# Kernel optimization log

Hardware: AMD Instinct MI355X
Metric: run time of the kernel (lower is better)

The kernel has to match this reference:

```python
import jax, jax.numpy as jnp
import numpy as np

B, S, D = 2, 2048, 1024
NH, HD = 16, 64
MLP = 4096
EPS = 1e-6  # flax nnx.RMSNorm default epsilon


def rms_norm(x, scale):
    var = jnp.mean(jnp.square(x.astype(jnp.float32)), axis=-1, keepdims=True)
    return (x * jax.lax.rsqrt(var + EPS)).astype(x.dtype) * scale


def setup_inputs() -> dict:
    key = jax.random.key(0)
    ks = jax.random.split(key, 16)
    lin = lambda k, fin, fout: jax.random.normal(k, (fin, fout), jnp.float32) / np.sqrt(fin)
    x = jax.random.normal(ks[0], (B, S, D), jnp.float32)
    # causal mask [b, s, s]
    mask = jnp.broadcast_to(jnp.tril(jnp.ones((S, S), jnp.bool_))[None], (B, S, S))
    return {
        "x": x,
        "mask": mask,
        "attn_norm_scale": jnp.ones((D,), jnp.float32),
        "q_w": lin(ks[1], D, D), "q_b": jnp.zeros((D,), jnp.float32),
        "k_w": lin(ks[2], D, D), "k_b": jnp.zeros((D,), jnp.float32),
        "v_w": lin(ks[3], D, D), "v_b": jnp.zeros((D,), jnp.float32),
        "o_w": lin(ks[4], D, D), "o_b": jnp.zeros((D,), jnp.float32),
        "ffn_norm_scale": jnp.ones((D,), jnp.float32),
        "gate_w": lin(ks[5], D, MLP), "gate_b": jnp.zeros((MLP,), jnp.float32),
        "up_w": lin(ks[6], D, MLP), "up_b": jnp.zeros((MLP,), jnp.float32),
        "down_w": lin(ks[7], MLP, D), "down_b": jnp.zeros((D,), jnp.float32),
    }


def reference(x, mask, attn_norm_scale, q_w, q_b, k_w, k_b, v_w, v_b, o_w, o_b,
              ffn_norm_scale, gate_w, gate_b, up_w, up_b, down_w, down_b):
    b, s, d = x.shape
    h = rms_norm(x, attn_norm_scale)
    q = (h @ q_w + q_b).reshape(b, s, NH, HD)
    k = (h @ k_w + k_b).reshape(b, s, NH, HD)
    v = (h @ v_w + v_b).reshape(b, s, NH, HD)
    scale = jnp.float32(HD) ** -0.5
    logits = jnp.einsum('bsnh,btnh->bnst', q, k) * scale  # [b, n, s, s]
    logits = jnp.where(mask[:, None, :, :], logits, jnp.finfo(logits.dtype).min)
    attn = jax.nn.softmax(logits.astype(jnp.float32), axis=-1).astype(x.dtype)
    attn_out = jnp.einsum('bnst,btnh->bsnh', attn, v).reshape(b, s, d)
    x = x + attn_out @ o_w + o_b
    h = rms_norm(x, ffn_norm_scale)
    ffn = (jax.nn.silu(h @ gate_w + gate_b) * (h @ up_w + up_b)) @ down_w + down_b
    return x + ffn
```

## Files before the change

kernel.cpp:

```cpp
#include <hip/hip_runtime.h>

#define S_LEN 2048
#define DMODEL 1024
#define NHEADS 16
#define MLPDIM 4096

typedef float f32x4 __attribute__((ext_vector_type(4)));
typedef __bf16 bf16x8 __attribute__((ext_vector_type(8)));
typedef __bf16 bf16x4 __attribute__((ext_vector_type(4)));

__device__ __forceinline__ void gload_lds16(const void* gsrc, void* ldst) {
  __builtin_amdgcn_global_load_lds(
      (const __attribute__((address_space(1))) void*)gsrc,
      (__attribute__((address_space(3))) void*)ldst, 16, 0, 0);
}

#define BARR() __builtin_amdgcn_s_barrier()
#define LGKM0() do { asm volatile("s_waitcnt lgkmcnt(0)" ::: "memory"); __builtin_amdgcn_sched_barrier(0); } while (0)
#define VMC(n) do { asm volatile("s_waitcnt vmcnt(" #n ")" ::: "memory"); __builtin_amdgcn_sched_barrier(0); } while (0)

__global__ __launch_bounds__(256) void transpose_cast64_k(
    const float* __restrict__ in, __bf16* __restrict__ out, int K, int N) {
  __shared__ __bf16 tile[64][66];
  int n0 = blockIdx.x * 64, k0 = blockIdx.y * 64;
  int t = threadIdx.x;
  int rr = (t & 63) >> 4, sl = t & 15, wv = t >> 6;
#pragma unroll
  for (int j = 0; j < 4; ++j) {
    int r = wv * 4 + rr + j * 16;
    f32x4 v = *(const f32x4*)(in + (size_t)(k0 + r) * N + n0 + sl * 4);
#pragma unroll
    for (int e = 0; e < 4; ++e) tile[r][sl * 4 + e] = (__bf16)v[e];
  }
  __syncthreads();
#pragma unroll
  for (int j = 0; j < 2; ++j) {
    int u = t + j * 256;
    int n = u >> 3, kc = u & 7;
    bf16x8 o;
#pragma unroll
    for (int e = 0; e < 8; ++e) o[e] = tile[kc * 8 + e][n];
    *(bf16x8*)(out + (size_t)(n0 + n) * K + k0 + kc * 8) = o;
  }
}

__global__ __launch_bounds__(256) void vtrans_k(
    const __bf16* __restrict__ qkv, __bf16* __restrict__ vt) {
  __shared__ __bf16 tile[32][33];
  int s0 = blockIdx.x * 32, c0 = blockIdx.y * 32, b = blockIdx.z;
  int tx = threadIdx.x & 31, ty = threadIdx.x >> 5;
#pragma unroll
  for (int r = 0; r < 32; r += 8)
    tile[r + ty][tx] = qkv[(size_t)(b * S_LEN + s0 + r + ty) * 3072 + 2048 + c0 + tx];
  __syncthreads();
#pragma unroll
  for (int r = 0; r < 32; r += 8)
    vt[(size_t)(b * 1024 + c0 + r + ty) * S_LEN + s0 + tx] = tile[tx][r + ty];
}

__global__ __launch_bounds__(256) void concat3_k(
    const float* __restrict__ a, const float* __restrict__ b,
    const float* __restrict__ c, float* __restrict__ dst) {
  int i = blockIdx.x * 256 + threadIdx.x;
  if (i < 1024) dst[i] = a[i];
  else if (i < 2048) dst[i] = b[i - 1024];
  else if (i < 3072) dst[i] = c[i - 2048];
}

__global__ __launch_bounds__(256) void rmsnorm_k(
    const float* __restrict__ x, const float* __restrict__ scale,
    __bf16* __restrict__ out) {
  int row = blockIdx.x, tid = threadIdx.x;
  f32x4 v = ((const f32x4*)(x + (size_t)row * DMODEL))[tid];
  float ss = v[0] * v[0] + v[1] * v[1] + v[2] * v[2] + v[3] * v[3];
#pragma unroll
  for (int off = 1; off < 64; off <<= 1) ss += __shfl_xor(ss, off, 64);
  __shared__ float part[4];
  if ((tid & 63) == 0) part[tid >> 6] = ss;
  __syncthreads();
  float tot = part[0] + part[1] + part[2] + part[3];
  float r = rsqrtf(tot * (1.0f / DMODEL) + 1e-6f);
  f32x4 s4 = ((const f32x4*)scale)[tid];
  bf16x4 o;
#pragma unroll
  for (int e = 0; e < 4; ++e) o[e] = (__bf16)(v[e] * r * s4[e]);
  ((bf16x4*)out)[(size_t)row * (DMODEL / 4) + tid] = o;
}

template <int OUT_BF16, int RESID, int SILU>
__global__ __launch_bounds__(512, 2) void gemm256(
    const __bf16* __restrict__ A, const __bf16* __restrict__ Bt,
    const float* __restrict__ bias, const float* __restrict__ resid,
    const __bf16* __restrict__ aux, void* __restrict__ Cout,
    int M, int N, int K) {
  __shared__ __attribute__((aligned(16))) __bf16 smA[2][256 * 32];
  __shared__ __attribute__((aligned(16))) __bf16 smB[2][256 * 32];
  int tid = threadIdx.x, lane = tid & 63, wave = tid >> 6;
  int l15 = lane & 15, g4 = lane >> 4;
  int wr = wave >> 2, wc = wave & 3;
  int lin = blockIdx.y * gridDim.x + blockIdx.x;
  int xcd = lin & 7, idx = lin >> 3;
  int bxl = idx >> 3, byl = idx & 7;
  int bn = ((xcd & 3) * 3 + bxl) * 256;
  int bm = ((xcd >> 2) * 8 + byl) * 256;
  const char* Ab = (const char*)(A + (size_t)bm * K);
  const char* Bb = (const char*)(Bt + (size_t)bn * K);
  int NT = K >> 5;

  f32x4 acc[8][4] = {};

  int o0 = tid * 16, o1 = tid * 16 + 8192;
  int r0s = o0 >> 6, c0s = o0 & 63;
  int r1s = o1 >> 6, c1s = o1 & 63;
  int cs0 = c0s ^ (((r0s >> 1) & 3) << 4);
  int cs1 = c1s ^ (((r1s >> 1) & 3) << 4);
  size_t K2 = (size_t)K * 2;

  auto stageA = [&](int t) {
    int b2 = t & 1;
    const char* g = Ab + (size_t)t * 64;
    gload_lds16(g + (size_t)r0s * K2 + cs0, (char*)&smA[b2][0] + o0);
    gload_lds16(g + (size_t)r1s * K2 + cs1, (char*)&smA[b2][0] + o1);
  };
  auto stageB = [&](int t) {
    int b2 = t & 1;
    const char* g = Bb + (size_t)t * 64;
    gload_lds16(g + (size_t)r0s * K2 + cs0, (char*)&smB[b2][0] + o0);
    gload_lds16(g + (size_t)r1s * K2 + cs1, (char*)&smB[b2][0] + o1);
  };
  auto rdA = [&](int b2, int r) -> bf16x8 {
    return *(const bf16x8*)((const char*)&smA[b2][0] + r * 64 + ((16 * g4) ^ (((r >> 1) & 3) << 4)));
  };
  auto rdB = [&](int b2, int r) -> bf16x8 {
    return *(const bf16x8*)((const char*)&smB[b2][0] + r * 64 + ((16 * g4) ^ (((r >> 1) & 3) << 4)));
  };

  stageA(0);
  stageB(0);
  stageB(1);
  VMC(2);
  BARR();

  for (int t = 0; t < NT; ++t) {
    int b2 = t & 1;
    bf16x8 af[4], bfr[4];
#pragma unroll
    for (int m = 0; m < 4; ++m) af[m] = rdA(b2, wr * 128 + m * 16 + l15);
#pragma unroll
    for (int n = 0; n < 4; ++n) bfr[n] = rdB(b2, wc * 64 + n * 16 + l15);
    if (t + 1 < NT) stageA(t + 1);
    BARR();
    LGKM0();
    __builtin_amdgcn_s_setprio(1);
#pragma unroll
    for (int m = 0; m < 4; ++m)
#pragma unroll
      for (int n = 0; n < 4; ++n)
        acc[m][n] = __builtin_amdgcn_mfma_f32_16x16x32_bf16(af[m], bfr[n], acc[m][n], 0, 0, 0);
    __builtin_amdgcn_s_setprio(0);
    BARR();
#pragma unroll
    for (int m = 0; m < 4; ++m) af[m] = rdA(b2, wr * 128 + 64 + m * 16 + l15);
    if (t + 2 < NT) stageB(t + 2);
    BARR();
    LGKM0();
    __builtin_amdgcn_s_setprio(1);
#pragma unroll
    for (int m = 0; m < 4; ++m)
#pragma unroll
      for (int n = 0; n < 4; ++n)
        acc[4 + m][n] = __builtin_amdgcn_mfma_f32_16x16x32_bf16(af[m], bfr[n], acc[4 + m][n], 0, 0, 0);
    __builtin_amdgcn_s_setprio(0);
    if (t < NT - 2) { VMC(2); }
    else if (t == NT - 2) { VMC(0); }
    BARR();
  }

  int r0 = bm + wr * 128 + g4 * 4;
  int c0 = bn + wc * 64 + l15;
#pragma unroll
  for (int n = 0; n < 4; ++n) {
    int c = c0 + n * 16;
    float bv = bias[c];
#pragma unroll
    for (int m = 0; m < 8; ++m) {
      int rb = r0 + m * 16;
#pragma unroll
      for (int rg = 0; rg < 4; ++rg) {
        int r = rb + rg;
        size_t idx2 = (size_t)r * N + c;
        float v = acc[m][n][rg] + bv;
        if (SILU) {
          float gg = (float)aux[idx2];
          v *= gg / (1.0f + __expf(-gg));
        }
        if (RESID) v += resid[idx2];
        if (OUT_BF16) ((__bf16*)Cout)[idx2] = (__bf16)v;
        else ((float*)Cout)[idx2] = v;
      }
    }
  }
}

__global__ __launch_bounds__(256, 4) void gemm_gu(
    const __bf16* __restrict__ A, const __bf16* __restrict__ Gt,
    const __bf16* __restrict__ Ut, const float* __restrict__ gb,
    const float* __restrict__ ub, __bf16* __restrict__ Cout,
    int M, int N, int K) {
  __shared__ __attribute__((aligned(16))) __bf16 As[128 * 64];
  __shared__ __attribute__((aligned(16))) __bf16 Gs[64 * 64];
  __shared__ __attribute__((aligned(16))) __bf16 Us[64 * 64];
  int tid = threadIdx.x, lane = tid & 63, wave = tid >> 6;
  int l15 = lane & 15, g4 = lane >> 4;
  int lin = blockIdx.x;
  int xcd = lin & 7, idx = lin >> 3;
  int bxl = idx >> 4, byl = idx & 15;
  int bn = ((xcd & 3) * 16 + bxl) * 64;
  int bm = ((xcd >> 2) * 16 + byl) * 128;
  int wr = wave >> 1, wc = wave & 1;
  f32x4 ag[4][2] = {}, au[4][2] = {};
  const __bf16* Abase = A + (size_t)bm * K;
  const __bf16* Gbase = Gt + (size_t)bn * K;
  const __bf16* Ubase = Ut + (size_t)bn * K;

  for (int k0 = 0; k0 < K; k0 += 64) {
#pragma unroll
    for (int j = 0; j < 4; ++j) {
      int u = tid + j * 256;
      int r = u >> 3, c = (u & 7) ^ (r & 7);
      gload_lds16(Abase + (size_t)r * K + k0 + c * 8, As + u * 8);
    }
#pragma unroll
    for (int j = 0; j < 2; ++j) {
      int u = tid + j * 256;
      int r = u >> 3, c = (u & 7) ^ (r & 7);
      gload_lds16(Gbase + (size_t)r * K + k0 + c * 8, Gs + u * 8);
      gload_lds16(Ubase + (size_t)r * K + k0 + c * 8, Us + u * 8);
    }
    __syncthreads();
#pragma unroll
    for (int ks = 0; ks < 2; ++ks) {
      bf16x8 af[4], gf[2], uf[2];
#pragma unroll
      for (int m = 0; m < 4; ++m) {
        int r = wr * 64 + m * 16 + l15;
        af[m] = *(const bf16x8*)(As + r * 64 + (((4 * ks + g4) ^ (r & 7)) << 3));
      }
#pragma unroll
      for (int n = 0; n < 2; ++n) {
        int r = wc * 32 + n * 16 + l15;
        int off = r * 64 + (((4 * ks + g4) ^ (r & 7)) << 3);
        gf[n] = *(const bf16x8*)(Gs + off);
        uf[n] = *(const bf16x8*)(Us + off);
      }
      __builtin_amdgcn_s_setprio(1);
#pragma unroll
      for (int m = 0; m < 4; ++m)
#pragma unroll
        for (int n = 0; n < 2; ++n) {
          ag[m][n] = __builtin_amdgcn_mfma_f32_16x16x32_bf16(af[m], gf[n], ag[m][n], 0, 0, 0);
          au[m][n] = __builtin_amdgcn_mfma_f32_16x16x32_bf16(af[m], uf[n], au[m][n], 0, 0, 0);
        }
      __builtin_amdgcn_s_setprio(0);
    }
    __syncthreads();
  }
  int r0 = bm + wr * 64 + g4 * 4;
  int c0 = bn + wc * 32 + l15;
#pragma unroll
  for (int n = 0; n < 2; ++n) {
    int c = c0 + n * 16;
    float gbv = gb[c], ubv = ub[c];
#pragma unroll
    for (int m = 0; m < 4; ++m) {
      int rb = r0 + m * 16;
#pragma unroll
      for (int rg = 0; rg < 4; ++rg) {
        float g = ag[m][n][rg] + gbv;
        float u = au[m][n][rg] + ubv;
        float v = g / (1.0f + __expf(-g)) * u;
        Cout[(size_t)(rb + rg) * N + c] = (__bf16)v;
      }
    }
  }
}

template <int OUT_BF16, int RESID, int SILU>
__global__ __launch_bounds__(256, 4) void gemm_n64(
    const __bf16* __restrict__ A, const __bf16* __restrict__ Bt,
    const float* __restrict__ bias, const float* __restrict__ resid,
    const __bf16* __restrict__ aux, void* __restrict__ Cout,
    int M, int N, int K) {
  __shared__ __attribute__((aligned(16))) __bf16 As[128 * 64];
  __shared__ __attribute__((aligned(16))) __bf16 Bs[64 * 64];
  int tid = threadIdx.x, lane = tid & 63, wave = tid >> 6;
  int l15 = lane & 15, g4 = lane >> 4;
  int nbx = gridDim.x;
  int lin = blockIdx.y * nbx + blockIdx.x;
  int nwg = nbx * gridDim.y;
  int qq = nwg >> 3;
  int wg = (lin & 7) * qq + (lin >> 3);
  int bn = (wg % nbx) * 64, bm = (wg / nbx) * 128;
  int wr = wave >> 1, wc = wave & 1;
  f32x4 acc[4][2] = {};
  const __bf16* Abase = A + (size_t)bm * K;
  const __bf16* Bbase = Bt + (size_t)bn * K;

  for (int k0 = 0; k0 < K; k0 += 64) {
#pragma unroll
    for (int i = 0; i < 4; ++i) {
      int u = tid + i * 256;
      int r = u >> 3, c = (u & 7) ^ (r & 7);
      gload_lds16(Abase + (size_t)r * K + k0 + c * 8, As + u * 8);
    }
#pragma unroll
    for (int i = 0; i < 2; ++i) {
      int u = tid + i * 256;
      int r = u >> 3, c = (u & 7) ^ (r & 7);
      gload_lds16(Bbase + (size_t)r * K + k0 + c * 8, Bs + u * 8);
    }
    __syncthreads();
#pragma unroll
    for (int ks = 0; ks < 2; ++ks) {
      bf16x8 af[4], bfr[2];
#pragma unroll
      for (int m = 0; m < 4; ++m) {
        int r = wr * 64 + m * 16 + l15;
        af[m] = *(const bf16x8*)(As + r * 64 + (((4 * ks + g4) ^ (r & 7)) << 3));
      }
#pragma unroll
      for (int n = 0; n < 2; ++n) {
        int r = wc * 32 + n * 16 + l15;
        bfr[n] = *(const bf16x8*)(Bs + r * 64 + (((4 * ks + g4) ^ (r & 7)) << 3));
      }
      __builtin_amdgcn_s_setprio(1);
#pragma unroll
      for (int m = 0; m < 4; ++m)
#pragma unroll
        for (int n = 0; n < 2; ++n)
          acc[m][n] = __builtin_amdgcn_mfma_f32_16x16x32_bf16(af[m], bfr[n], acc[m][n], 0, 0, 0);
      __builtin_amdgcn_s_setprio(0);
    }
    __syncthreads();
  }
  int r0 = bm + wr * 64 + g4 * 4;
  int c0 = bn + wc * 32 + l15;
#pragma unroll
  for (int n = 0; n < 2; ++n) {
    int c = c0 + n * 16;
    float bv = bias[c];
#pragma unroll
    for (int m = 0; m < 4; ++m) {
      int rb = r0 + m * 16;
#pragma unroll
      for (int rg = 0; rg < 4; ++rg) {
        int r = rb + rg;
        size_t idx = (size_t)r * N + c;
        float v = acc[m][n][rg] + bv;
        if (SILU) {
          float gg = (float)aux[idx];
          v *= gg / (1.0f + __expf(-gg));
        }
        if (RESID) v += resid[idx];
        if (OUT_BF16) ((__bf16*)Cout)[idx] = (__bf16)v;
        else ((float*)Cout)[idx] = v;
      }
    }
  }
}

#define SCL2E 0.180336879f
__global__ __launch_bounds__(512, 4) void attn_k(
    const __bf16* __restrict__ qkv, const __bf16* __restrict__ vt,
    __bf16* __restrict__ ao) {
  __shared__ __attribute__((aligned(16))) __bf16 Ks[2][128 * 64];
  __shared__ __attribute__((aligned(16))) __bf16 Vs[2][64 * 128];
  int tid = threadIdx.x, lane = tid & 63, w = tid >> 6;
  int l15 = lane & 15, g4 = lane >> 4;
  int bh = blockIdx.x, b = bh >> 4, h = bh & 15;
  int qt = 15 - blockIdx.y;
  int qb = qt * 128;
  int qw = qb + w * 16;
  const __bf16* qkvb = qkv + (size_t)b * S_LEN * 3072 + h * 64;
  const __bf16* kgb = qkvb + 1024;
  const __bf16* vtb = vt + (size_t)b * 1024 * S_LEN + (size_t)(h * 64) * S_LEN;

  bf16x8 qf[2];
#pragma unroll
  for (int ks = 0; ks < 2; ++ks)
    qf[ks] = *(const bf16x8*)(qkvb + (size_t)(qw + l15) * 3072 + 32 * ks + 8 * g4);

  f32x4 oa[4] = {};
  float mrow = -1e30f, lrow = 0.f;
  int q = qw + l15;
  int nt = qt + 1;

  auto stage = [&](int kvb, int buf) {
#pragma unroll
    for (int i = 0; i < 2; ++i) {
      int u = tid + i * 512;
      int r = u >> 3, c = u & 7;
      gload_lds16(kgb + (size_t)(kvb + r) * 3072 + ((c ^ (r & 7)) << 3),
                  Ks[buf] + w * 512 + i * 4096);
    }
#pragma unroll
    for (int i = 0; i < 2; ++i) {
      int u = tid + i * 512;
      int r = u >> 4, cu = u & 15;
      gload_lds16(vtb + (size_t)r * S_LEN + kvb + ((cu ^ (r & 7)) << 3),
                  Vs[buf] + w * 512 + i * 4096);
    }
  };

  stage(0, 0);
  __syncthreads();
  int buf = 0;
  for (int t = 0; t < nt; ++t) {
    int kvb = t * 128;
    if (t + 1 < nt) stage(kvb + 128, buf ^ 1);

    f32x4 sa[8];
#pragma unroll
    for (int i = 0; i < 8; ++i) sa[i] = f32x4{0.f, 0.f, 0.f, 0.f};
#pragma unroll
    for (int st = 0; st < 2; ++st)
#pragma unroll
      for (int ks = 0; ks < 2; ++ks) {
        bf16x8 kf[4];
#pragma unroll
        for (int n = 0; n < 4; ++n) {
          int rr = st * 64 + n * 16 + l15;
          int bc = (64 * ks + 16 * g4) ^ ((rr & 7) << 4);
          kf[n] = *(const bf16x8*)((const char*)Ks[buf] + rr * 128 + bc);
        }
        __builtin_amdgcn_s_setprio(1);
#pragma unroll
        for (int n = 0; n < 4; ++n)
          sa[st * 4 + n] = __builtin_amdgcn_mfma_f32_16x16x32_bf16(kf[n], qf[ks], sa[st * 4 + n], 0, 0, 0);
        __builtin_amdgcn_s_setprio(0);
      }

    bool lastt = (t == nt - 1);
    float nmx = -1e30f;
#pragma unroll
    for (int i = 0; i < 8; ++i)
#pragma unroll
      for (int rg = 0; rg < 4; ++rg) {
        float s = sa[i][rg] * SCL2E;
        if (lastt) {
          int key = kvb + (i >> 2) * 64 + (i & 3) * 16 + 4 * g4 + rg;
          s = (key <= q) ? s : -1e30f;
        }
        sa[i][rg] = s;
        nmx = fmaxf(nmx, s);
      }
    nmx = fmaxf(nmx, __shfl_xor(nmx, 16));
    nmx = fmaxf(nmx, __shfl_xor(nmx, 32));
    float nm = fmaxf(mrow, nmx);
    float sc = exp2f(mrow - nm);
    mrow = nm;
    float rs = 0.f;
    bf16x8 pa[2][2];
#pragma unroll
    for (int st = 0; st < 2; ++st)
#pragma unroll
      for (int ks = 0; ks < 2; ++ks)
#pragma unroll
        for (int hf = 0; hf < 2; ++hf)
#pragma unroll
          for (int rg = 0; rg < 4; ++rg) {
            float p = exp2f(sa[st * 4 + 2 * ks + hf][rg] - nm);
            rs += p;
            pa[st][ks][hf * 4 + rg] = (__bf16)p;
          }
    rs += __shfl_xor(rs, 16);
    rs += __shfl_xor(rs, 32);
    lrow = lrow * sc + rs;
#pragma unroll
    for (int rg = 0; rg < 4; ++rg) {
      float scq = __shfl(sc, 4 * g4 + rg);
#pragma unroll
      for (int dn = 0; dn < 4; ++dn) oa[dn][rg] *= scq;
    }

#pragma unroll
    for (int st = 0; st < 2; ++st)
#pragma unroll
      for (int ks = 0; ks < 2; ++ks) {
        __builtin_amdgcn_s_setprio(1);
#pragma unroll
        for (int dn = 0; dn < 4; ++dn) {
          int rr = dn * 16 + l15;
          int swz = (rr & 7) << 4;
          int bb = st * 128 + 64 * ks + 8 * g4;
          const char* vrow = (const char*)Vs[buf] + rr * 256;
          bf16x4 v0 = *(const bf16x4*)(vrow + (bb ^ swz));
          bf16x4 v1 = *(const bf16x4*)(vrow + ((bb + 32) ^ swz));
          bf16x8 vf;
          vf[0] = v0[0]; vf[1] = v0[1]; vf[2] = v0[2]; vf[3] = v0[3];
          vf[4] = v1[0]; vf[5] = v1[1]; vf[6] = v1[2]; vf[7] = v1[3];
          oa[dn] = __builtin_amdgcn_mfma_f32_16x16x32_bf16(pa[st][ks], vf, oa[dn], 0, 0, 0);
        }
        __builtin_amdgcn_s_setprio(0);
      }
    __syncthreads();
    buf ^= 1;
  }

  __bf16* aobase = ao + (size_t)b * S_LEN * DMODEL + h * 64;
#pragma unroll
  for (int rg = 0; rg < 4; ++rg) {
    float rl = 1.0f / __shfl(lrow, 4 * g4 + rg);
    int qo = qw + 4 * g4 + rg;
#pragma unroll
    for (int dn = 0; dn < 4; ++dn)
      aobase[(size_t)qo * DMODEL + dn * 16 + l15] = (__bf16)(oa[dn][rg] * rl);
  }
}

#define OFF_WQKV 0
#define OFF_WO 6291456
#define OFF_WG 8388608
#define OFF_WU 16777216
#define OFF_WD 25165824
#define OFF_BQKV 33554432
#define OFF_H 33570816
#define OFF_QKV 41959424
#define OFF_AO 67125248
#define OFF_T 75513856
#define OFF_VT OFF_T
#define OFF_X2 109068288

extern "C" void kernel_launch(void* const* d_in, const int* in_sizes, int n_in,
                              void* d_out, int out_size, void* d_ws, size_t ws_size,
                              hipStream_t stream) {
  (void)in_sizes; (void)n_in; (void)out_size; (void)ws_size;
  const float* x = (const float*)d_in[0];
  const float* attn_scale = (const float*)d_in[2];
  const float* q_w = (const float*)d_in[3];
  const float* q_b = (const float*)d_in[4];
  const float* k_w = (const float*)d_in[5];
  const float* k_b = (const float*)d_in[6];
  const float* v_w = (const float*)d_in[7];
  const float* v_b = (const float*)d_in[8];
  const float* o_w = (const float*)d_in[9];
  const float* o_b = (const float*)d_in[10];
  const float* ffn_scale = (const float*)d_in[11];
  const float* gate_w = (const float*)d_in[12];
  const float* gate_b = (const float*)d_in[13];
  const float* up_w = (const float*)d_in[14];
  const float* up_b = (const float*)d_in[15];
  const float* down_w = (const float*)d_in[16];
  const float* down_b = (const float*)d_in[17];

  char* ws = (char*)d_ws;
  __bf16* wqkv = (__bf16*)(ws + OFF_WQKV);
  __bf16* wo = (__bf16*)(ws + OFF_WO);
  __bf16* wg = (__bf16*)(ws + OFF_WG);
  __bf16* wu = (__bf16*)(ws + OFF_WU);
  __bf16* wd = (__bf16*)(ws + OFF_WD);
  float* bqkv = (float*)(ws + OFF_BQKV);
  __bf16* hbuf = (__bf16*)(ws + OFF_H);
  __bf16* qkvbuf = (__bf16*)(ws + OFF_QKV);
  __bf16* aobuf = (__bf16*)(ws + OFF_AO);
  __bf16* tbuf = (__bf16*)(ws + OFF_T);
  __bf16* vtbuf = (__bf16*)(ws + OFF_VT);
  float* x2 = (float*)(ws + OFF_X2);

  dim3 blk(256);
  transpose_cast64_k<<<dim3(16, 16), blk, 0, stream>>>(q_w, wqkv, 1024, 1024);
  transpose_cast64_k<<<dim3(16, 16), blk, 0, stream>>>(k_w, wqkv + 1024 * 1024, 1024, 1024);
  transpose_cast64_k<<<dim3(16, 16), blk, 0, stream>>>(v_w, wqkv + 2 * 1024 * 1024, 1024, 1024);
  transpose_cast64_k<<<dim3(16, 16), blk, 0, stream>>>(o_w, wo, 1024, 1024);
  transpose_cast64_k<<<dim3(64, 16), blk, 0, stream>>>(gate_w, wg, 1024, 4096);
  transpose_cast64_k<<<dim3(64, 16), blk, 0, stream>>>(up_w, wu, 1024, 4096);
  transpose_cast64_k<<<dim3(16, 64), blk, 0, stream>>>(down_w, wd, 4096, 1024);
  concat3_k<<<12, blk, 0, stream>>>(q_b, k_b, v_b, bqkv);
  rmsnorm_k<<<4096, blk, 0, stream>>>(x, attn_scale, hbuf);
  gemm256<1, 0, 0><<<dim3(12, 16), dim3(512), 0, stream>>>(hbuf, wqkv, bqkv, nullptr, nullptr, qkvbuf, 4096, 3072, 1024);
  vtrans_k<<<dim3(64, 32, 2), blk, 0, stream>>>(qkvbuf, vtbuf);
  attn_k<<<dim3(32, 16), dim3(512), 0, stream>>>(qkvbuf, vtbuf, aobuf);
  gemm_n64<0, 1, 0><<<dim3(16, 32), blk, 0, stream>>>(aobuf, wo, o_b, x, nullptr, x2, 4096, 1024, 1024);
  rmsnorm_k<<<4096, blk, 0, stream>>>(x2, ffn_scale, hbuf);
  gemm_gu<<<dim3(2048), blk, 0, stream>>>(hbuf, wg, wu, gate_b, up_b, tbuf, 4096, 4096, 1024);
  gemm_n64<0, 1, 0><<<dim3(16, 32), blk, 0, stream>>>(tbuf, wd, down_b, x2, nullptr, (float*)d_out, 4096, 1024, 4096);
}
```

Baseline: 273.6 us.

## Double-buffer LDS in small GEMMs, drop gemm256, remap blocks per XCD

Adds double-buffered LDS staging to gemm_gu and gemm_n64, so the next K tile's global-to-LDS loads overlap the current tile's MFMA work, with vmcnt waits instead of a full syncthreads. Occupancy hints drop (4 to 2 and 3) because LDS use doubles. The 256x256 gemm256 kernel is removed and the QKV projection now uses gemm_n64 with 128x64 tiles. gemm_n64 switches to a 1D grid with an XCD-aware mapping that keeps contiguous row blocks on one XCD. The tradeoff is fewer resident waves and smaller QKV tiles with less data reuse.

Measured after the change: 284.0 us. 3.8% more time.

```diff
diff --git a/kernel.cpp b/kernel.cpp
--- a/kernel.cpp
+++ b/kernel.cpp
@@ -16,7 +16,6 @@
 }
 
 #define BARR() __builtin_amdgcn_s_barrier()
-#define LGKM0() do { asm volatile("s_waitcnt lgkmcnt(0)" ::: "memory"); __builtin_amdgcn_sched_barrier(0); } while (0)
 #define VMC(n) do { asm volatile("s_waitcnt vmcnt(" #n ")" ::: "memory"); __builtin_amdgcn_sched_barrier(0); } while (0)
 
 __global__ __launch_bounds__(256) void transpose_cast64_k(
@@ -87,129 +86,14 @@
   ((bf16x4*)out)[(size_t)row * (DMODEL / 4) + tid] = o;
 }
 
-template <int OUT_BF16, int RESID, int SILU>
-__global__ __launch_bounds__(512, 2) void gemm256(
-    const __bf16* __restrict__ A, const __bf16* __restrict__ Bt,
-    const float* __restrict__ bias, const float* __restrict__ resid,
-    const __bf16* __restrict__ aux, void* __restrict__ Cout,
-    int M, int N, int K) {
-  __shared__ __attribute__((aligned(16))) __bf16 smA[2][256 * 32];
-  __shared__ __attribute__((aligned(16))) __bf16 smB[2][256 * 32];
-  int tid = threadIdx.x, lane = tid & 63, wave = tid >> 6;
-  int l15 = lane & 15, g4 = lane >> 4;
-  int wr = wave >> 2, wc = wave & 3;
-  int lin = blockIdx.y * gridDim.x + blockIdx.x;
-  int xcd = lin & 7, idx = lin >> 3;
-  int bxl = idx >> 3, byl = idx & 7;
-  int bn = ((xcd & 3) * 3 + bxl) * 256;
-  int bm = ((xcd >> 2) * 8 + byl) * 256;
-  const char* Ab = (const char*)(A + (size_t)bm * K);
-  const char* Bb = (const char*)(Bt + (size_t)bn * K);
-  int NT = K >> 5;
-
-  f32x4 acc[8][4] = {};
-
-  int o0 = tid * 16, o1 = tid * 16 + 8192;
-  int r0s = o0 >> 6, c0s = o0 & 63;
-  int r1s = o1 >> 6, c1s = o1 & 63;
-  int cs0 = c0s ^ (((r0s >> 1) & 3) << 4);
-  int cs1 = c1s ^ (((r1s >> 1) & 3) << 4);
-  size_t K2 = (size_t)K * 2;
-
-  auto stageA = [&](int t) {
-    int b2 = t & 1;
-    const char* g = Ab + (size_t)t * 64;
-    gload_lds16(g + (size_t)r0s * K2 + cs0, (char*)&smA[b2][0] + o0);
-    gload_lds16(g + (size_t)r1s * K2 + cs1, (char*)&smA[b2][0] + o1);
-  };
-  auto stageB = [&](int t) {
-    int b2 = t & 1;
-    const char* g = Bb + (size_t)t * 64;
-    gload_lds16(g + (size_t)r0s * K2 + cs0, (char*)&smB[b2][0] + o0);
-    gload_lds16(g + (size_t)r1s * K2 + cs1, (char*)&smB[b2][0] + o1);
-  };
-  auto rdA = [&](int b2, int r) -> bf16x8 {
-    return *(const bf16x8*)((const char*)&smA[b2][0] + r * 64 + ((16 * g4) ^ (((r >> 1) & 3) << 4)));
-  };
-  auto rdB = [&](int b2, int r) -> bf16x8 {
-    return *(const bf16x8*)((const char*)&smB[b2][0] + r * 64 + ((16 * g4) ^ (((r >> 1) & 3) << 4)));
-  };
-
-  stageA(0);
-  stageB(0);
-  stageB(1);
-  VMC(2);
-  BARR();
-
-  for (int t = 0; t < NT; ++t) {
-    int b2 = t & 1;
-    bf16x8 af[4], bfr[4];
-#pragma unroll
-    for (int m = 0; m < 4; ++m) af[m] = rdA(b2, wr * 128 + m * 16 + l15);
-#pragma unroll
-    for (int n = 0; n < 4; ++n) bfr[n] = rdB(b2, wc * 64 + n * 16 + l15);
-    if (t + 1 < NT) stageA(t + 1);
-    BARR();
-    LGKM0();
-    __builtin_amdgcn_s_setprio(1);
-#pragma unroll
-    for (int m = 0; m < 4; ++m)
-#pragma unroll
-      for (int n = 0; n < 4; ++n)
-        acc[m][n] = __builtin_amdgcn_mfma_f32_16x16x32_bf16(af[m], bfr[n], acc[m][n], 0, 0, 0);
-    __builtin_amdgcn_s_setprio(0);
-    BARR();
-#pragma unroll
-    for (int m = 0; m < 4; ++m) af[m] = rdA(b2, wr * 128 + 64 + m * 16 + l15);
-    if (t + 2 < NT) stageB(t + 2);
-    BARR();
-    LGKM0();
-    __builtin_amdgcn_s_setprio(1);
-#pragma unroll
-    for (int m = 0; m < 4; ++m)
-#pragma unroll
-      for (int n = 0; n < 4; ++n)
-        acc[4 + m][n] = __builtin_amdgcn_mfma_f32_16x16x32_bf16(af[m], bfr[n], acc[4 + m][n], 0, 0, 0);
-    __builtin_amdgcn_s_setprio(0);
-    if (t < NT - 2) { VMC(2); }
-    else if (t == NT - 2) { VMC(0); }
-    BARR();
-  }
-
-  int r0 = bm + wr * 128 + g4 * 4;
-  int c0 = bn + wc * 64 + l15;
-#pragma unroll
-  for (int n = 0; n < 4; ++n) {
-    int c = c0 + n * 16;
-    float bv = bias[c];
-#pragma unroll
-    for (int m = 0; m < 8; ++m) {
-      int rb = r0 + m * 16;
-#pragma unroll
-      for (int rg = 0; rg < 4; ++rg) {
-        int r = rb + rg;
-        size_t idx2 = (size_t)r * N + c;
-        float v = acc[m][n][rg] + bv;
-        if (SILU) {
-          float gg = (float)aux[idx2];
-          v *= gg / (1.0f + __expf(-gg));
-        }
-        if (RESID) v += resid[idx2];
-        if (OUT_BF16) ((__bf16*)Cout)[idx2] = (__bf16)v;
-        else ((float*)Cout)[idx2] = v;
-      }
-    }
-  }
-}
-
-__global__ __launch_bounds__(256, 4) void gemm_gu(
+__global__ __launch_bounds__(256, 2) void gemm_gu(
     const __bf16* __restrict__ A, const __bf16* __restrict__ Gt,
     const __bf16* __restrict__ Ut, const float* __restrict__ gb,
     const float* __restrict__ ub, __bf16* __restrict__ Cout,
     int M, int N, int K) {
-  __shared__ __attribute__((aligned(16))) __bf16 As[128 * 64];
-  __shared__ __attribute__((aligned(16))) __bf16 Gs[64 * 64];
-  __shared__ __attribute__((aligned(16))) __bf16 Us[64 * 64];
+  __shared__ __attribute__((aligned(16))) __bf16 As[2][128 * 64];
+  __shared__ __attribute__((aligned(16))) __bf16 Gs[2][64 * 64];
+  __shared__ __attribute__((aligned(16))) __bf16 Us[2][64 * 64];
   int tid = threadIdx.x, lane = tid & 63, wave = tid >> 6;
   int l15 = lane & 15, g4 = lane >> 4;
   int lin = blockIdx.x;
@@ -223,35 +107,43 @@
   const __bf16* Gbase = Gt + (size_t)bn * K;
   const __bf16* Ubase = Ut + (size_t)bn * K;
 
-  for (int k0 = 0; k0 < K; k0 += 64) {
+  auto stage = [&](int k0, int sb) {
 #pragma unroll
     for (int j = 0; j < 4; ++j) {
       int u = tid + j * 256;
       int r = u >> 3, c = (u & 7) ^ (r & 7);
-      gload_lds16(Abase + (size_t)r * K + k0 + c * 8, As + u * 8);
+      gload_lds16(Abase + (size_t)r * K + k0 + c * 8, As[sb] + u * 8);
     }
 #pragma unroll
     for (int j = 0; j < 2; ++j) {
       int u = tid + j * 256;
       int r = u >> 3, c = (u & 7) ^ (r & 7);
-      gload_lds16(Gbase + (size_t)r * K + k0 + c * 8, Gs + u * 8);
-      gload_lds16(Ubase + (size_t)r * K + k0 + c * 8, Us + u * 8);
-    }
-    __syncthreads();
+      gload_lds16(Gbase + (size_t)r * K + k0 + c * 8, Gs[sb] + u * 8);
+      gload_lds16(Ubase + (size_t)r * K + k0 + c * 8, Us[sb] + u * 8);
+    }
+  };
+
+  int NT = K >> 6;
+  stage(0, 0);
+  for (int t = 0; t < NT; ++t) {
+    int sb = t & 1;
+    if (t + 1 < NT) { stage((t + 1) << 6, sb ^ 1); VMC(8); }
+    else { VMC(0); }
+    BARR();
 #pragma unroll
     for (int ks = 0; ks < 2; ++ks) {
       bf16x8 af[4], gf[2], uf[2];
 #pragma unroll
       for (int m = 0; m < 4; ++m) {
         int r = wr * 64 + m * 16 + l15;
-        af[m] = *(const bf16x8*)(As + r * 64 + (((4 * ks + g4) ^ (r & 7)) << 3));
+        af[m] = *(const bf16x8*)(As[sb] + r * 64 + (((4 * ks + g4) ^ (r & 7)) << 3));
       }
 #pragma unroll
       for (int n = 0; n < 2; ++n) {
         int r = wc * 32 + n * 16 + l15;
         int off = r * 64 + (((4 * ks + g4) ^ (r & 7)) << 3);
-        gf[n] = *(const bf16x8*)(Gs + off);
-        uf[n] = *(const bf16x8*)(Us + off);
+        gf[n] = *(const bf16x8*)(Gs[sb] + off);
+        uf[n] = *(const bf16x8*)(Us[sb] + off);
       }
       __builtin_amdgcn_s_setprio(1);
 #pragma unroll
@@ -263,7 +155,7 @@
         }
       __builtin_amdgcn_s_setprio(0);
     }
-    __syncthreads();
+    BARR();
   }
   int r0 = bm + wr * 64 + g4 * 4;
   int c0 = bn + wc * 32 + l15;
@@ -286,52 +178,58 @@
 }
 
 template <int OUT_BF16, int RESID, int SILU>
-__global__ __launch_bounds__(256, 4) void gemm_n64(
+__global__ __launch_bounds__(256, 3) void gemm_n64(
     const __bf16* __restrict__ A, const __bf16* __restrict__ Bt,
     const float* __restrict__ bias, const float* __restrict__ resid,
     const __bf16* __restrict__ aux, void* __restrict__ Cout,
     int M, int N, int K) {
-  __shared__ __attribute__((aligned(16))) __bf16 As[128 * 64];
-  __shared__ __attribute__((aligned(16))) __bf16 Bs[64 * 64];
+  __shared__ __attribute__((aligned(16))) __bf16 As[2][128 * 64];
+  __shared__ __attribute__((aligned(16))) __bf16 Bs[2][64 * 64];
   int tid = threadIdx.x, lane = tid & 63, wave = tid >> 6;
   int l15 = lane & 15, g4 = lane >> 4;
-  int nbx = gridDim.x;
-  int lin = blockIdx.y * nbx + blockIdx.x;
-  int nwg = nbx * gridDim.y;
-  int qq = nwg >> 3;
-  int wg = (lin & 7) * qq + (lin >> 3);
-  int bn = (wg % nbx) * 64, bm = (wg / nbx) * 128;
+  int npx = M >> 10;
+  int xcd = blockIdx.x & 7, j = blockIdx.x >> 3;
+  int bm = (xcd * npx + (j % npx)) * 128;
+  int bn = (j / npx) * 64;
   int wr = wave >> 1, wc = wave & 1;
   f32x4 acc[4][2] = {};
   const __bf16* Abase = A + (size_t)bm * K;
   const __bf16* Bbase = Bt + (size_t)bn * K;
 
-  for (int k0 = 0; k0 < K; k0 += 64) {
+  auto stage = [&](int k0, int sb) {
 #pragma unroll
     for (int i = 0; i < 4; ++i) {
       int u = tid + i * 256;
       int r = u >> 3, c = (u & 7) ^ (r & 7);
-      gload_lds16(Abase + (size_t)r * K + k0 + c * 8, As + u * 8);
+      gload_lds16(Abase + (size_t)r * K + k0 + c * 8, As[sb] + u * 8);
     }
 #pragma unroll
     for (int i = 0; i < 2; ++i) {
       int u = tid + i * 256;
       int r = u >> 3, c = (u & 7) ^ (r & 7);
-      gload_lds16(Bbase + (size_t)r * K + k0 + c * 8, Bs + u * 8);
-    }
-    __syncthreads();
+      gload_lds16(Bbase + (size_t)r * K + k0 + c * 8, Bs[sb] + u * 8);
+    }
+  };
+
+  int NT = K >> 6;
+  stage(0, 0);
+  for (int t = 0; t < NT; ++t) {
+    int sb = t & 1;
+    if (t + 1 < NT) { stage((t + 1) << 6, sb ^ 1); VMC(6); }
+    else { VMC(0); }
+    BARR();
 #pragma unroll
     for (int ks = 0; ks < 2; ++ks) {
       bf16x8 af[4], bfr[2];
 #pragma unroll
       for (int m = 0; m < 4; ++m) {
         int r = wr * 64 + m * 16 + l15;
-        af[m] = *(const bf16x8*)(As + r * 64 + (((4 * ks + g4) ^ (r & 7)) << 3));
+        af[m] = *(const bf16x8*)(As[sb] + r * 64 + (((4 * ks + g4) ^ (r & 7)) << 3));
       }
 #pragma unroll
       for (int n = 0; n < 2; ++n) {
         int r = wc * 32 + n * 16 + l15;
-        bfr[n] = *(const bf16x8*)(Bs + r * 64 + (((4 * ks + g4) ^ (r & 7)) << 3));
+        bfr[n] = *(const bf16x8*)(Bs[sb] + r * 64 + (((4 * ks + g4) ^ (r & 7)) << 3));
       }
       __builtin_amdgcn_s_setprio(1);
 #pragma unroll
@@ -341,7 +239,7 @@
           acc[m][n] = __builtin_amdgcn_mfma_f32_16x16x32_bf16(af[m], bfr[n], acc[m][n], 0, 0, 0);
       __builtin_amdgcn_s_setprio(0);
     }
-    __syncthreads();
+    BARR();
   }
   int r0 = bm + wr * 64 + g4 * 4;
   int c0 = bn + wc * 32 + l15;
@@ -577,11 +475,11 @@
   transpose_cast64_k<<<dim3(16, 64), blk, 0, stream>>>(down_w, wd, 4096, 1024);
   concat3_k<<<12, blk, 0, stream>>>(q_b, k_b, v_b, bqkv);
   rmsnorm_k<<<4096, blk, 0, stream>>>(x, attn_scale, hbuf);
-  gemm256<1, 0, 0><<<dim3(12, 16), dim3(512), 0, stream>>>(hbuf, wqkv, bqkv, nullptr, nullptr, qkvbuf, 4096, 3072, 1024);
+  gemm_n64<1, 0, 0><<<dim3(1536), blk, 0, stream>>>(hbuf, wqkv, bqkv, nullptr, nullptr, qkvbuf, 4096, 3072, 1024);
   vtrans_k<<<dim3(64, 32, 2), blk, 0, stream>>>(qkvbuf, vtbuf);
   attn_k<<<dim3(32, 16), dim3(512), 0, stream>>>(qkvbuf, vtbuf, aobuf);
-  gemm_n64<0, 1, 0><<<dim3(16, 32), blk, 0, stream>>>(aobuf, wo, o_b, x, nullptr, x2, 4096, 1024, 1024);
+  gemm_n64<0, 1, 0><<<dim3(512), blk, 0, stream>>>(aobuf, wo, o_b, x, nullptr, x2, 4096, 1024, 1024);
   rmsnorm_k<<<4096, blk, 0, stream>>>(x2, ffn_scale, hbuf);
   gemm_gu<<<dim3(2048), blk, 0, stream>>>(hbuf, wg, wu, gate_b, up_b, tbuf, 4096, 4096, 1024);
-  gemm_n64<0, 1, 0><<<dim3(16, 32), blk, 0, stream>>>(tbuf, wd, down_b, x2, nullptr, (float*)d_out, 4096, 1024, 4096);
-}
+  gemm_n64<0, 1, 0><<<dim3(512), blk, 0, stream>>>(tbuf, wd, down_b, x2, nullptr, (float*)d_out, 4096, 1024, 4096);
+}
```
